# Kernel optimization log

Measured on AMD Instinct MI355X. Metric: run time of the kernel, lower is better.

The kernel has to match this reference:

```python
import jax, jax.numpy as jnp
import numpy as np

EPS = 1e-5  # layernorm epsilon


def _fp8_roundtrip(t):
    """Emulate per-tensor FP8 (E4M3) cast with scale=1 (initial TE scaling state):
    quantize to float8_e4m3 and dequantize back. amax tracking does not change
    first-iteration numerics since scale_inv == 1."""
    return t.astype(jnp.float8_e4m3fn).astype(jnp.float32)


def setup_inputs() -> dict:
    key = jax.random.key(0)
    k1, k2 = jax.random.split(key)
    tokens, hidden, units = 65536, 768, 768
    x = jax.random.normal(k1, (tokens, hidden), dtype=jnp.float32)
    gamma = jnp.ones((hidden,), dtype=jnp.float32)
    beta = jnp.zeros((hidden,), dtype=jnp.float32)
    # kaiming-ish scale so fp8 dynamic range is exercised sanely
    kernel = jax.random.normal(k2, (hidden, units), dtype=jnp.float32) * (1.0 / np.sqrt(hidden))
    bias = jnp.zeros((units,), dtype=jnp.float32)
    return {"x": x, "gamma": gamma, "beta": beta, "kernel": kernel, "bias": bias}


def reference(x, gamma, beta, kernel, bias):
    # --- fused LayerNorm (tex.layernorm_fwd_fp8): per-row mu/rsigma over hidden dim ---
    mu = jnp.mean(x, axis=-1, keepdims=True)
    var = jnp.mean(jnp.square(x - mu), axis=-1, keepdims=True)
    rsigma = jax.lax.rsqrt(var + EPS)
    ln_out = (x - mu) * rsigma * gamma + beta  # [tokens, hidden]

    # --- FP8 cast of activations and weight (scale=1 initial state) ---
    ln_q = _fp8_roundtrip(ln_out)
    k_q = _fp8_roundtrip(kernel)

    # --- te_gemm: fp8 GEMM with fp32 accumulation + bias fusion ---
    out = jnp.matmul(ln_q, k_q, preferred_element_type=jnp.float32) + bias
    return out
```

## Files before the change

### kernel.cpp

```cpp
#include <hip/hip_runtime.h>
#include <stdint.h>

typedef float f32x4 __attribute__((ext_vector_type(4)));
typedef long i64;

#define HID 768
#define UNITS 768
#define BM 64
#define BN 384
#define LDS_STRIDE 776
#define NFRAG 6
#define MFRAG 4
#define KK_STEPS 24
#define NPKT (48 * 24)

__device__ __forceinline__ uint8_t f32_to_e4m3_sw(float x) {
    uint32_t u;
    __builtin_memcpy(&u, &x, 4);
    uint32_t sign = (u >> 24) & 0x80u;
    uint32_t a = u & 0x7fffffffu;
    if (a > 0x43e00000u) return (uint8_t)(sign | 0x7e);
    if (a < 0x3c800000u) {
        float s;
        __builtin_memcpy(&s, &a, 4);
        int q = (int)rintf(s * 512.0f);
        return (uint8_t)(sign | (uint32_t)q);
    }
    uint32_t e = a >> 23;
    uint32_t m = a & 0x7fffffu;
    uint32_t mant = m >> 20;
    uint32_t rest = m & 0xfffffu;
    mant += (rest > 0x80000u) || (rest == 0x80000u && (mant & 1u));
    uint32_t te = e - 127u + 7u;
    if (mant == 8u) { mant = 0u; te += 1u; }
    return (uint8_t)(sign | (te << 3) | mant);
}

__device__ __forceinline__ uint32_t pack4_e4m3(float a, float b, float c, float d) {
#if __has_builtin(__builtin_amdgcn_cvt_pk_fp8_f32)
    int v = 0;
    v = __builtin_amdgcn_cvt_pk_fp8_f32(a, b, v, false);
    v = __builtin_amdgcn_cvt_pk_fp8_f32(c, d, v, true);
    return (uint32_t)v;
#else
    return (uint32_t)f32_to_e4m3_sw(a) | ((uint32_t)f32_to_e4m3_sw(b) << 8) |
           ((uint32_t)f32_to_e4m3_sw(c) << 16) | ((uint32_t)f32_to_e4m3_sw(d) << 24);
#endif
}

__global__ void pack_b_kernel(const float* __restrict__ K, uint8_t* __restrict__ Bp) {
    const int lane = threadIdx.x & 63;
    const int wid = (int)((blockIdx.x * blockDim.x + threadIdx.x) >> 6);
    if (wid >= NPKT) return;
    const int fn = wid / KK_STEPS, kk = wid % KK_STEPS;
    const int n = fn * 16 + (lane & 15);
    const int k0 = kk * 32 + (lane >> 4) * 8;
    float v[8];
#pragma unroll
    for (int j = 0; j < 8; ++j) v[j] = K[(size_t)(k0 + j) * UNITS + n];
    uint2 pr;
    pr.x = pack4_e4m3(v[0], v[1], v[2], v[3]);
    pr.y = pack4_e4m3(v[4], v[5], v[6], v[7]);
    *(uint2*)(Bp + ((size_t)wid << 9) + (size_t)lane * 8) = pr;
}

__global__ __launch_bounds__(256, 3)
void fused_ln_gemm(const float* __restrict__ x,
                   const float* __restrict__ gamma,
                   const float* __restrict__ beta,
                   const uint8_t* __restrict__ Bp,
                   const float* __restrict__ bias,
                   float* __restrict__ out) {
    __shared__ uint8_t Alds[BM * LDS_STRIDE];
    const int tid = threadIdx.x;
    const int lane = tid & 63;
    const int wave = tid >> 6;
    const int bid = (int)blockIdx.x;
    const int ny = bid & 1;
    const int mt = bid >> 1;
    const int row0 = mt * BM;

    for (int rr = 0; rr < BM / 4; ++rr) {
        const int row = wave * (BM / 4) + rr;
        const float4* xr = (const float4*)(x + (size_t)(row0 + row) * HID);
        float4 v[3];
        float s = 0.f, s2 = 0.f;
#pragma unroll
        for (int i = 0; i < 3; ++i) {
            v[i] = xr[i * 64 + lane];
            s  += v[i].x + v[i].y + v[i].z + v[i].w;
            s2 += v[i].x * v[i].x + v[i].y * v[i].y + v[i].z * v[i].z + v[i].w * v[i].w;
        }
#pragma unroll
        for (int off = 32; off; off >>= 1) {
            s  += __shfl_xor(s, off);
            s2 += __shfl_xor(s2, off);
        }
        const float mu = s * (1.0f / HID);
        const float var = fmaxf(s2 * (1.0f / HID) - mu * mu, 0.0f);
        const float rs = rsqrtf(var + 1e-5f);
#pragma unroll
        for (int i = 0; i < 3; ++i) {
            const int c4 = i * 64 + lane;
            const float4 g  = ((const float4*)gamma)[c4];
            const float4 bb = ((const float4*)beta)[c4];
            const float y0 = (v[i].x - mu) * rs * g.x + bb.x;
            const float y1 = (v[i].y - mu) * rs * g.y + bb.y;
            const float y2 = (v[i].z - mu) * rs * g.z + bb.z;
            const float y3 = (v[i].w - mu) * rs * g.w + bb.w;
            *(uint32_t*)&Alds[row * LDS_STRIDE + c4 * 4] = pack4_e4m3(y0, y1, y2, y3);
        }
    }
    __syncthreads();

    const int nl = lane & 15, quad = lane >> 4;
    f32x4 acc[MFRAG][NFRAG];
#pragma unroll
    for (int mf = 0; mf < MFRAG; ++mf)
#pragma unroll
        for (int f = 0; f < NFRAG; ++f) acc[mf][f] = (f32x4){0.f, 0.f, 0.f, 0.f};

    const uint8_t* ap[MFRAG];
#pragma unroll
    for (int mf = 0; mf < MFRAG; ++mf)
        ap[mf] = &Alds[(mf * 16 + nl) * LDS_STRIDE + quad * 8];

    const i64* Bq = (const i64*)Bp;
    const int fn0 = ny * 24 + wave * NFRAG;

    i64 bcur[NFRAG];
#pragma unroll
    for (int f = 0; f < NFRAG; ++f)
        bcur[f] = Bq[(size_t)((fn0 + f) * KK_STEPS) * 64 + lane];

#pragma unroll 4
    for (int kk = 0; kk < KK_STEPS; ++kk) {
        const int kn = (kk + 1 < KK_STEPS) ? kk + 1 : kk;
        i64 bnxt[NFRAG];
#pragma unroll
        for (int f = 0; f < NFRAG; ++f)
            bnxt[f] = Bq[(size_t)((fn0 + f) * KK_STEPS + kn) * 64 + lane];

        i64 a[MFRAG];
#pragma unroll
        for (int mf = 0; mf < MFRAG; ++mf)
            a[mf] = *(const i64*)(ap[mf] + kk * 32);

#pragma unroll
        for (int f = 0; f < NFRAG; ++f)
#pragma unroll
            for (int mf = 0; mf < MFRAG; ++mf)
                acc[mf][f] = __builtin_amdgcn_mfma_f32_16x16x32_fp8_fp8(a[mf], bcur[f], acc[mf][f], 0, 0, 0);

#pragma unroll
        for (int f = 0; f < NFRAG; ++f) bcur[f] = bnxt[f];
    }

#pragma unroll
    for (int f = 0; f < NFRAG; ++f) {
        const int col = ny * BN + wave * 96 + f * 16 + nl;
        const float bv = bias[col];
#pragma unroll
        for (int mf = 0; mf < MFRAG; ++mf) {
            const int row = row0 + mf * 16 + quad * 4;
            float* o = out + (size_t)row * UNITS + col;
            o[0 * UNITS] = acc[mf][f][0] + bv;
            o[1 * UNITS] = acc[mf][f][1] + bv;
            o[2 * UNITS] = acc[mf][f][2] + bv;
            o[3 * UNITS] = acc[mf][f][3] + bv;
        }
    }
}

extern "C" void kernel_launch(void* const* d_in, const int* in_sizes, int n_in,
                              void* d_out, int out_size, void* d_ws, size_t ws_size,
                              hipStream_t stream) {
    const float* x     = (const float*)d_in[0];
    const float* gamma = (const float*)d_in[1];
    const float* beta  = (const float*)d_in[2];
    const float* kern  = (const float*)d_in[3];
    const float* bias  = (const float*)d_in[4];
    float* out = (float*)d_out;
    uint8_t* Bp = (uint8_t*)d_ws;
    const int tokens = in_sizes[0] / HID;

    hipLaunchKernelGGL(pack_b_kernel, dim3((NPKT * 64 + 255) / 256), dim3(256), 0, stream,
                       kern, Bp);
    hipLaunchKernelGGL(fused_ln_gemm, dim3((tokens / BM) * 2), dim3(256), 0, stream,
                       x, gamma, beta, Bp, bias, out);
}
```

Baseline: 408.9 us.

## Split LayerNorm+FP8 pack into separate kernel feeding a fragment-packed GEMM

Replaces the fused LN+GEMM kernel with two kernels. The first normalizes rows, quantizes them to FP8 and writes A in MFMA-fragment order to workspace. The second streams pre-packed A and B fragments straight from global memory into registers, with no LDS and with prefetch. This removes the LN work duplicated across the two N-halves, since the old kernel read x twice, and frees the LDS stage in the GEMM. The cost is an extra 48 MB FP8 round trip through memory and one more launch. The fused path is kept as a fallback when the workspace is too small.

```diff
diff --git a/kernel.cpp b/kernel.cpp
--- a/kernel.cpp
+++ b/kernel.cpp
@@ -62,6 +62,145 @@
     pr.x = pack4_e4m3(v[0], v[1], v[2], v[3]);
     pr.y = pack4_e4m3(v[4], v[5], v[6], v[7]);
     *(uint2*)(Bp + ((size_t)wid << 9) + (size_t)lane * 8) = pr;
+}
+
+__global__ __launch_bounds__(256, 4)
+void ln_pack_a(const float* __restrict__ x,
+               const float* __restrict__ gamma,
+               const float* __restrict__ beta,
+               uint8_t* __restrict__ Ap) {
+    __shared__ uint8_t Alds[16 * LDS_STRIDE];
+    const int tid = threadIdx.x;
+    const int lane = tid & 63;
+    const int wave = tid >> 6;
+    const int frag = (int)blockIdx.x;
+    const int row0 = frag * 16 + wave * 4;
+
+    float4 g[3], bb[3];
+#pragma unroll
+    for (int i = 0; i < 3; ++i) {
+        g[i]  = ((const float4*)gamma)[i * 64 + lane];
+        bb[i] = ((const float4*)beta )[i * 64 + lane];
+    }
+
+    float4 v[4][3];
+    float s[4], s2[4];
+#pragma unroll
+    for (int r = 0; r < 4; ++r) {
+        const float4* xr = (const float4*)(x + (size_t)(row0 + r) * HID);
+        s[r] = 0.f; s2[r] = 0.f;
+#pragma unroll
+        for (int i = 0; i < 3; ++i) {
+            const float4 t = xr[i * 64 + lane];
+            v[r][i] = t;
+            s[r]  += t.x + t.y + t.z + t.w;
+            s2[r] += t.x * t.x + t.y * t.y + t.z * t.z + t.w * t.w;
+        }
+    }
+#pragma unroll
+    for (int off = 32; off; off >>= 1) {
+#pragma unroll
+        for (int r = 0; r < 4; ++r) {
+            s[r]  += __shfl_xor(s[r], off);
+            s2[r] += __shfl_xor(s2[r], off);
+        }
+    }
+#pragma unroll
+    for (int r = 0; r < 4; ++r) {
+        const float mu = s[r] * (1.0f / HID);
+        const float var = fmaxf(s2[r] * (1.0f / HID) - mu * mu, 0.0f);
+        const float rs = rsqrtf(var + 1e-5f);
+#pragma unroll
+        for (int i = 0; i < 3; ++i) {
+            const int c4 = i * 64 + lane;
+            const float y0 = (v[r][i].x - mu) * rs * g[i].x + bb[i].x;
+            const float y1 = (v[r][i].y - mu) * rs * g[i].y + bb[i].y;
+            const float y2 = (v[r][i].z - mu) * rs * g[i].z + bb[i].z;
+            const float y3 = (v[r][i].w - mu) * rs * g[i].w + bb[i].w;
+            *(uint32_t*)&Alds[(wave * 4 + r) * LDS_STRIDE + c4 * 4] = pack4_e4m3(y0, y1, y2, y3);
+        }
+    }
+    __syncthreads();
+
+    const int nl = lane & 15, quad = lane >> 4;
+#pragma unroll
+    for (int t = 0; t < KK_STEPS / 4; ++t) {
+        const int kk = wave * (KK_STEPS / 4) + t;
+        const i64 val = *(const i64*)&Alds[nl * LDS_STRIDE + quad * 8 + kk * 32];
+        ((i64*)Ap)[((size_t)frag * KK_STEPS + kk) * 64 + lane] = val;
+    }
+}
+
+__global__ __launch_bounds__(256, 3)
+void gemm_packed(const uint8_t* __restrict__ Ap,
+                 const uint8_t* __restrict__ Bp,
+                 const float* __restrict__ bias,
+                 float* __restrict__ out) {
+    const int tid = threadIdx.x;
+    const int lane = tid & 63;
+    const int wave = tid >> 6;
+    const int bid = (int)blockIdx.x;
+    const int ny = bid & 1;
+    const int mt = bid >> 1;
+    const int row0 = mt * BM;
+    const int nl = lane & 15, quad = lane >> 4;
+
+    f32x4 acc[MFRAG][NFRAG];
+#pragma unroll
+    for (int mf = 0; mf < MFRAG; ++mf)
+#pragma unroll
+        for (int f = 0; f < NFRAG; ++f) acc[mf][f] = (f32x4){0.f, 0.f, 0.f, 0.f};
+
+    const i64* Aq = (const i64*)Ap;
+    const i64* Bq = (const i64*)Bp;
+    const int fn0 = ny * 24 + wave * NFRAG;
+    const size_t abase = (size_t)(mt * MFRAG) * KK_STEPS * 64 + lane;
+
+    i64 acur[MFRAG], bcur[NFRAG];
+#pragma unroll
+    for (int mf = 0; mf < MFRAG; ++mf)
+        acur[mf] = Aq[abase + (size_t)mf * KK_STEPS * 64];
+#pragma unroll
+    for (int f = 0; f < NFRAG; ++f)
+        bcur[f] = Bq[(size_t)((fn0 + f) * KK_STEPS) * 64 + lane];
+
+#pragma unroll 2
+    for (int kk = 0; kk < KK_STEPS; ++kk) {
+        const int kn = (kk + 1 < KK_STEPS) ? kk + 1 : kk;
+        i64 anxt[MFRAG], bnxt[NFRAG];
+#pragma unroll
+        for (int mf = 0; mf < MFRAG; ++mf)
+            anxt[mf] = Aq[abase + ((size_t)mf * KK_STEPS + kn) * 64];
+#pragma unroll
+        for (int f = 0; f < NFRAG; ++f)
+            bnxt[f] = Bq[(size_t)((fn0 + f) * KK_STEPS + kn) * 64 + lane];
+
+#pragma unroll
+        for (int f = 0; f < NFRAG; ++f)
+#pragma unroll
+            for (int mf = 0; mf < MFRAG; ++mf)
+                acc[mf][f] = __builtin_amdgcn_mfma_f32_16x16x32_fp8_fp8(acur[mf], bcur[f], acc[mf][f], 0, 0, 0);
+
+#pragma unroll
+        for (int mf = 0; mf < MFRAG; ++mf) acur[mf] = anxt[mf];
+#pragma unroll
+        for (int f = 0; f < NFRAG; ++f) bcur[f] = bnxt[f];
+    }
+
+#pragma unroll
+    for (int f = 0; f < NFRAG; ++f) {
+        const int col = ny * BN + wave * 96 + f * 16 + nl;
+        const float bv = bias[col];
+#pragma unroll
+        for (int mf = 0; mf < MFRAG; ++mf) {
+            const int row = row0 + mf * 16 + quad * 4;
+            float* o = out + (size_t)row * UNITS + col;
+            o[0 * UNITS] = acc[mf][f][0] + bv;
+            o[1 * UNITS] = acc[mf][f][1] + bv;
+            o[2 * UNITS] = acc[mf][f][2] + bv;
+            o[3 * UNITS] = acc[mf][f][3] + bv;
+        }
+    }
 }
 
 __global__ __launch_bounds__(256, 3)
@@ -181,11 +320,23 @@
     const float* kern  = (const float*)d_in[3];
     const float* bias  = (const float*)d_in[4];
     float* out = (float*)d_out;
+    const int tokens = in_sizes[0] / HID;
+
     uint8_t* Bp = (uint8_t*)d_ws;
-    const int tokens = in_sizes[0] / HID;
+    const size_t bp_bytes = (size_t)NPKT * 512;
+    const size_t ap_bytes = (size_t)tokens * HID;
 
     hipLaunchKernelGGL(pack_b_kernel, dim3((NPKT * 64 + 255) / 256), dim3(256), 0, stream,
                        kern, Bp);
-    hipLaunchKernelGGL(fused_ln_gemm, dim3((tokens / BM) * 2), dim3(256), 0, stream,
-                       x, gamma, beta, Bp, bias, out);
-}
+
+    if (ws_size >= bp_bytes + ap_bytes) {
+        uint8_t* Ap = Bp + bp_bytes;
+        hipLaunchKernelGGL(ln_pack_a, dim3(tokens / 16), dim3(256), 0, stream,
+                           x, gamma, beta, Ap);
+        hipLaunchKernelGGL(gemm_packed, dim3((tokens / BM) * 2), dim3(256), 0, stream,
+                           Ap, Bp, bias, out);
+    } else {
+        hipLaunchKernelGGL(fused_ln_gemm, dim3((tokens / BM) * 2), dim3(256), 0, stream,
+                           x, gamma, beta, Bp, bias, out);
+    }
+}
```

Result: slower. 417.5 us (+2.1%).

## Compute LayerNorm once per row tile and loop over both N halves

Applied to the files above, without the earlier changes.

Each block now handles one 64-row tile and loops over both 384-column halves, so the LayerNorm and FP8 packing of x happen once instead of twice. This halves the x reads and LN work. The LN phase also batches four rows per wave with gamma/beta hoisted into registers, which adds memory-level parallelism. MFMA sections are wrapped in s_setprio and outputs use nontemporal stores. The cost is half as many blocks, a serialized second GEMM pass per block, and occupancy lowered from 3 to 2 blocks per CU.

```diff
diff --git a/kernel.cpp b/kernel.cpp
--- a/kernel.cpp
+++ b/kernel.cpp
@@ -64,110 +64,130 @@
     *(uint2*)(Bp + ((size_t)wid << 9) + (size_t)lane * 8) = pr;
 }
 
-__global__ __launch_bounds__(256, 3)
-void fused_ln_gemm(const float* __restrict__ x,
-                   const float* __restrict__ gamma,
-                   const float* __restrict__ beta,
-                   const uint8_t* __restrict__ Bp,
-                   const float* __restrict__ bias,
-                   float* __restrict__ out) {
+__global__ __launch_bounds__(256, 2)
+void fused_ln_gemm_v2(const float* __restrict__ x,
+                      const float* __restrict__ gamma,
+                      const float* __restrict__ beta,
+                      const uint8_t* __restrict__ Bp,
+                      const float* __restrict__ bias,
+                      float* __restrict__ out) {
     __shared__ uint8_t Alds[BM * LDS_STRIDE];
     const int tid = threadIdx.x;
     const int lane = tid & 63;
     const int wave = tid >> 6;
-    const int bid = (int)blockIdx.x;
-    const int ny = bid & 1;
-    const int mt = bid >> 1;
+    const int mt = (int)blockIdx.x;
     const int row0 = mt * BM;
 
-    for (int rr = 0; rr < BM / 4; ++rr) {
-        const int row = wave * (BM / 4) + rr;
-        const float4* xr = (const float4*)(x + (size_t)(row0 + row) * HID);
-        float4 v[3];
-        float s = 0.f, s2 = 0.f;
-#pragma unroll
-        for (int i = 0; i < 3; ++i) {
-            v[i] = xr[i * 64 + lane];
-            s  += v[i].x + v[i].y + v[i].z + v[i].w;
-            s2 += v[i].x * v[i].x + v[i].y * v[i].y + v[i].z * v[i].z + v[i].w * v[i].w;
+    float4 g[3], bbv[3];
+#pragma unroll
+    for (int i = 0; i < 3; ++i) {
+        g[i]   = ((const float4*)gamma)[i * 64 + lane];
+        bbv[i] = ((const float4*)beta )[i * 64 + lane];
+    }
+#pragma unroll
+    for (int b = 0; b < 4; ++b) {
+        const int lrow0 = wave * 16 + b * 4;
+        float4 v[4][3];
+        float s[4], s2[4];
+#pragma unroll
+        for (int r = 0; r < 4; ++r) {
+            const float4* xr = (const float4*)(x + (size_t)(row0 + lrow0 + r) * HID);
+            s[r] = 0.f; s2[r] = 0.f;
+#pragma unroll
+            for (int i = 0; i < 3; ++i) {
+                const float4 t = xr[i * 64 + lane];
+                v[r][i] = t;
+                s[r]  += t.x + t.y + t.z + t.w;
+                s2[r] += t.x * t.x + t.y * t.y + t.z * t.z + t.w * t.w;
+            }
         }
 #pragma unroll
         for (int off = 32; off; off >>= 1) {
-            s  += __shfl_xor(s, off);
-            s2 += __shfl_xor(s2, off);
-        }
-        const float mu = s * (1.0f / HID);
-        const float var = fmaxf(s2 * (1.0f / HID) - mu * mu, 0.0f);
-        const float rs = rsqrtf(var + 1e-5f);
-#pragma unroll
-        for (int i = 0; i < 3; ++i) {
-            const int c4 = i * 64 + lane;
-            const float4 g  = ((const float4*)gamma)[c4];
-            const float4 bb = ((const float4*)beta)[c4];
-            const float y0 = (v[i].x - mu) * rs * g.x + bb.x;
-            const float y1 = (v[i].y - mu) * rs * g.y + bb.y;
-            const float y2 = (v[i].z - mu) * rs * g.z + bb.z;
-            const float y3 = (v[i].w - mu) * rs * g.w + bb.w;
-            *(uint32_t*)&Alds[row * LDS_STRIDE + c4 * 4] = pack4_e4m3(y0, y1, y2, y3);
+#pragma unroll
+            for (int r = 0; r < 4; ++r) {
+                s[r]  += __shfl_xor(s[r], off);
+                s2[r] += __shfl_xor(s2[r], off);
+            }
+        }
+#pragma unroll
+        for (int r = 0; r < 4; ++r) {
+            const float mu = s[r] * (1.0f / HID);
+            const float var = fmaxf(s2[r] * (1.0f / HID) - mu * mu, 0.0f);
+            const float rs = rsqrtf(var + 1e-5f);
+#pragma unroll
+            for (int i = 0; i < 3; ++i) {
+                const int c4 = i * 64 + lane;
+                const float y0 = (v[r][i].x - mu) * rs * g[i].x + bbv[i].x;
+                const float y1 = (v[r][i].y - mu) * rs * g[i].y + bbv[i].y;
+                const float y2 = (v[r][i].z - mu) * rs * g[i].z + bbv[i].z;
+                const float y3 = (v[r][i].w - mu) * rs * g[i].w + bbv[i].w;
+                *(uint32_t*)&Alds[(lrow0 + r) * LDS_STRIDE + c4 * 4] =
+                    pack4_e4m3(y0, y1, y2, y3);
+            }
         }
     }
     __syncthreads();
 
     const int nl = lane & 15, quad = lane >> 4;
-    f32x4 acc[MFRAG][NFRAG];
-#pragma unroll
-    for (int mf = 0; mf < MFRAG; ++mf)
-#pragma unroll
-        for (int f = 0; f < NFRAG; ++f) acc[mf][f] = (f32x4){0.f, 0.f, 0.f, 0.f};
-
     const uint8_t* ap[MFRAG];
 #pragma unroll
     for (int mf = 0; mf < MFRAG; ++mf)
         ap[mf] = &Alds[(mf * 16 + nl) * LDS_STRIDE + quad * 8];
-
     const i64* Bq = (const i64*)Bp;
-    const int fn0 = ny * 24 + wave * NFRAG;
-
-    i64 bcur[NFRAG];
-#pragma unroll
-    for (int f = 0; f < NFRAG; ++f)
-        bcur[f] = Bq[(size_t)((fn0 + f) * KK_STEPS) * 64 + lane];
+
+    for (int ny = 0; ny < 2; ++ny) {
+        f32x4 acc[MFRAG][NFRAG];
+#pragma unroll
+        for (int mf = 0; mf < MFRAG; ++mf)
+#pragma unroll
+            for (int f = 0; f < NFRAG; ++f) acc[mf][f] = (f32x4){0.f, 0.f, 0.f, 0.f};
+
+        const int fn0 = ny * 24 + wave * NFRAG;
+
+        i64 bcur[NFRAG];
+#pragma unroll
+        for (int f = 0; f < NFRAG; ++f)
+            bcur[f] = Bq[(size_t)((fn0 + f) * KK_STEPS) * 64 + lane];
 
 #pragma unroll 4
-    for (int kk = 0; kk < KK_STEPS; ++kk) {
-        const int kn = (kk + 1 < KK_STEPS) ? kk + 1 : kk;
-        i64 bnxt[NFRAG];
-#pragma unroll
-        for (int f = 0; f < NFRAG; ++f)
-            bnxt[f] = Bq[(size_t)((fn0 + f) * KK_STEPS + kn) * 64 + lane];
-
-        i64 a[MFRAG];
-#pragma unroll
-        for (int mf = 0; mf < MFRAG; ++mf)
-            a[mf] = *(const i64*)(ap[mf] + kk * 32);
-
-#pragma unroll
-        for (int f = 0; f < NFRAG; ++f)
+        for (int kk = 0; kk < KK_STEPS; ++kk) {
+            const int kn = (kk + 1 < KK_STEPS) ? kk + 1 : kk;
+            i64 bnxt[NFRAG];
+#pragma unroll
+            for (int f = 0; f < NFRAG; ++f)
+                bnxt[f] = Bq[(size_t)((fn0 + f) * KK_STEPS + kn) * 64 + lane];
+
+            i64 a[MFRAG];
 #pragma unroll
             for (int mf = 0; mf < MFRAG; ++mf)
-                acc[mf][f] = __builtin_amdgcn_mfma_f32_16x16x32_fp8_fp8(a[mf], bcur[f], acc[mf][f], 0, 0, 0);
-
-#pragma unroll
-        for (int f = 0; f < NFRAG; ++f) bcur[f] = bnxt[f];
-    }
-
-#pragma unroll
-    for (int f = 0; f < NFRAG; ++f) {
-        const int col = ny * BN + wave * 96 + f * 16 + nl;
-        const float bv = bias[col];
-#pragma unroll
-        for (int mf = 0; mf < MFRAG; ++mf) {
-            const int row = row0 + mf * 16 + quad * 4;
-            float* o = out + (size_t)row * UNITS + col;
-            o[0 * UNITS] = acc[mf][f][0] + bv;
-            o[1 * UNITS] = acc[mf][f][1] + bv;
-            o[2 * UNITS] = acc[mf][f][2] + bv;
-            o[3 * UNITS] = acc[mf][f][3] + bv;
+                a[mf] = *(const i64*)(ap[mf] + kk * 32);
+
+            __builtin_amdgcn_s_setprio(1);
+#pragma unroll
+            for (int f = 0; f < NFRAG; ++f)
+#pragma unroll
+                for (int mf = 0; mf < MFRAG; ++mf)
+                    acc[mf][f] = __builtin_amdgcn_mfma_f32_16x16x32_fp8_fp8(
+                        a[mf], bcur[f], acc[mf][f], 0, 0, 0);
+            __builtin_amdgcn_s_setprio(0);
+
+#pragma unroll
+            for (int f = 0; f < NFRAG; ++f) bcur[f] = bnxt[f];
+        }
+
+#pragma unroll
+        for (int f = 0; f < NFRAG; ++f) {
+            const int col = ny * BN + wave * 96 + f * 16 + nl;
+            const float bv = bias[col];
+#pragma unroll
+            for (int mf = 0; mf < MFRAG; ++mf) {
+                const int row = row0 + mf * 16 + quad * 4;
+                float* o = out + (size_t)row * UNITS + col;
+                __builtin_nontemporal_store(acc[mf][f][0] + bv, o + 0 * UNITS);
+                __builtin_nontemporal_store(acc[mf][f][1] + bv, o + 1 * UNITS);
+                __builtin_nontemporal_store(acc[mf][f][2] + bv, o + 2 * UNITS);
+                __builtin_nontemporal_store(acc[mf][f][3] + bv, o + 3 * UNITS);
+            }
         }
     }
 }
@@ -186,6 +206,6 @@
 
     hipLaunchKernelGGL(pack_b_kernel, dim3((NPKT * 64 + 255) / 256), dim3(256), 0, stream,
                        kern, Bp);
-    hipLaunchKernelGGL(fused_ln_gemm, dim3((tokens / BM) * 2), dim3(256), 0, stream,
+    hipLaunchKernelGGL(fused_ln_gemm_v2, dim3(tokens / BM), dim3(256), 0, stream,
                        x, gamma, beta, Bp, bias, out);
 }
```

Measured after the change: 385.7 us. 1.06x faster.
